# Performance work log

Hardware: AMD Instinct MI355X
Metric: run time of the kernel (lower is better)

## Reference

```python
import jax, jax.numpy as jnp
import numpy as np

THRESHOLD = 1.0
TAU_H, TAU_O = 50.0, 30.0

def setup_inputs() -> dict:
    key = jax.random.key(0)
    k1, k2, k3, k4, k5, k6 = jax.random.split(key, 6)
    B, T, S, H = 2048, 1024, 64, 256
    return {
        "sensor_history": jax.random.uniform(k1, (B, T, S), dtype=jnp.float32),
        "noise": jax.random.uniform(k2, (B, T, S), dtype=jnp.float32),
        "W_h": jax.random.normal(k3, (H, S), dtype=jnp.float32) * (1.0 / np.sqrt(S)),
        "b_h": jax.random.normal(k4, (H,), dtype=jnp.float32) * 0.01,
        "W_o": jax.random.normal(k5, (1, H), dtype=jnp.float32) * (1.0 / np.sqrt(H)),
        "b_o": jax.random.normal(k6, (1,), dtype=jnp.float32) * 0.01,
    }

def reference(sensor_history, noise, W_h, b_h, W_o, b_o):
    B, T, S = sensor_history.shape
    beta_h = jnp.exp(jnp.float32(-1.0 / TAU_H))  # membrane decay, hidden
    beta_o = jnp.exp(jnp.float32(-1.0 / TAU_O))  # membrane decay, output

    def step(carry, xs):
        v_h, v_o, acc = carry
        sensor_t, noise_t = xs  # (B, S) each
        # stochastic rate coding: spike if uniform < sensor value
        spikes_in = (noise_t < sensor_t).astype(jnp.float32)
        # hidden LIF: leaky integrate, threshold, hard reset
        v_h = beta_h * v_h + spikes_in @ W_h.T + b_h
        s_h = (v_h >= THRESHOLD).astype(jnp.float32)
        v_h = v_h * (1.0 - s_h)
        # output LIF
        v_o = beta_o * v_o + s_h @ W_o.T + b_o
        s_o = (v_o >= THRESHOLD).astype(jnp.float32)
        v_o = v_o * (1.0 - s_o)
        return (v_h, v_o, acc + s_o), None

    v_h0 = jnp.zeros((B, W_h.shape[0]), dtype=jnp.float32)
    v_o0 = jnp.zeros((B, 1), dtype=jnp.float32)
    acc0 = jnp.zeros((B, 1), dtype=jnp.float32)
    # time-major scan over the recurrence
    xs = (jnp.swapaxes(sensor_history, 0, 1), jnp.swapaxes(noise, 0, 1))
    (_, _, acc), _ = jax.lax.scan(step, (v_h0, v_o0, acc0), xs)
    return acc / jnp.float32(T)
```

## Files before the change

### kernel.cpp

```cpp
#include <hip/hip_runtime.h>

#define TT 1024
#define SS 64
#define HH 256
#define BB 4
#define TC 16
#define NC (TT / TC)

typedef _Float16 f16x8 __attribute__((ext_vector_type(8)));
typedef float    f32x4 __attribute__((ext_vector_type(4)));
typedef unsigned int u32x4 __attribute__((ext_vector_type(4)));

template <int CTRL>
__device__ __forceinline__ float dpp_add(float x) {
    int v = __float_as_int(x);
    int m = __builtin_amdgcn_update_dpp(v, v, CTRL, 0xF, 0xF, true);
    return x + __int_as_float(m);
}
__device__ __forceinline__ float wxsum_row(float x) {
    x = dpp_add<0x124>(x);
    x = dpp_add<0x128>(x);
    return x;
}

__device__ __forceinline__ float rowsum16_asm(float x) {
    float a, b, c, d;
    asm("s_nop 1\n\t"
        "v_add_f32_dpp %0, %1, %1 quad_perm:[1,0,3,2] row_mask:0xf bank_mask:0xf"
        : "=v"(a) : "v"(x));
    asm("s_nop 1\n\t"
        "v_add_f32_dpp %0, %1, %1 quad_perm:[2,3,0,1] row_mask:0xf bank_mask:0xf"
        : "=v"(b) : "v"(a));
    asm("s_nop 1\n\t"
        "v_add_f32_dpp %0, %1, %1 row_half_mirror row_mask:0xf bank_mask:0xf"
        : "=v"(c) : "v"(b));
    asm("s_nop 1\n\t"
        "v_add_f32_dpp %0, %1, %1 row_mirror row_mask:0xf bank_mask:0xf"
        : "=v"(d) : "v"(c));
    return d;
}

__launch_bounds__(512, 4)
__global__ void snn_fused(const float* __restrict__ sensor,
                          const float* __restrict__ noise,
                          const float* __restrict__ Wh,
                          const float* __restrict__ bh,
                          const float* __restrict__ Wo,
                          const float* __restrict__ bo,
                          float* __restrict__ out)
{
    __shared__ __align__(16) char  spk[2][4 * 16 * 128];
    __shared__ __align__(16) float rpart[2][BB][8][TC];

    const int tid  = threadIdx.x;
    const int lane = tid & 63;
    const int wave = tid >> 6;
    const int b0   = blockIdx.x * BB;

    f16x8 whi[2][2], wlo[2][2];
    #pragma unroll
    for (int nti = 0; nti < 2; ++nti) {
        const int h = (wave + nti * 8) * 16 + (lane & 15);
        #pragma unroll
        for (int kh = 0; kh < 2; ++kh) {
            const int k = kh * 32 + (lane >> 4) * 8;
            const float* p = Wh + (size_t)h * SS + k;
            float4 wa = *(const float4*)(p);
            float4 wb = *(const float4*)(p + 4);
            float wv[8] = {wa.x, wa.y, wa.z, wa.w, wb.x, wb.y, wb.z, wb.w};
            f16x8 fh, fl;
            #pragma unroll
            for (int j = 0; j < 8; ++j) {
                _Float16 hi = (_Float16)wv[j];
                float r1 = wv[j] - (float)hi;
                fh[j] = hi;
                fl[j] = (_Float16)(r1 * 2048.0f);
            }
            whi[nti][kh] = fh; wlo[nti][kh] = fl;
        }
    }

    const int hc = lane & 15;
    const float bh0 = bh[wave * 16 + hc], bh1 = bh[128 + wave * 16 + hc];
    const float wo0 = Wo[wave * 16 + hc], wo1 = Wo[128 + wave * 16 + hc];
    const float bov = bo[0];
    const float betah = expf(-1.0f / 50.0f);
    const float betao = expf(-1.0f / 30.0f);

    const f32x4 zero4 = {0.0f, 0.0f, 0.0f, 0.0f};

    float vh0 = 0.0f, vh1 = 0.0f;
    float vo = 0.0f, acc = 0.0f;

    const int wtw  = tid >> 7;
    const int wm   = (tid >> 3) & 15;
    const int woct = tid & 7;
    const int wrow = wtw * 16 + wm;
    const int wbyte = wrow * 128 + ((woct * 16) ^ ((wrow & 7) << 4));
    const float* sgp = sensor + ((size_t)(b0 + (wm >> 2)) * TT + wtw * 4 + (wm & 3)) * SS + woct * 8;
    const float* ngp = noise  + ((size_t)(b0 + (wm >> 2)) * TT + wtw * 4 + (wm & 3)) * SS + woct * 8;

    float4 sA, sB, nA, nB;

    auto pack_spk = [&](char* dst) {
        u32x4 sv;
        sv[0] = (nA.x < sA.x ? 0x3C00u : 0u) | (nA.y < sA.y ? 0x3C000000u : 0u);
        sv[1] = (nA.z < sA.z ? 0x3C00u : 0u) | (nA.w < sA.w ? 0x3C000000u : 0u);
        sv[2] = (nB.x < sB.x ? 0x3C00u : 0u) | (nB.y < sB.y ? 0x3C000000u : 0u);
        sv[3] = (nB.z < sB.z ? 0x3C00u : 0u) | (nB.w < sB.w ? 0x3C000000u : 0u);
        *(u32x4*)(dst + wbyte) = sv;
    };

    auto p4_step = [&](const float (*rp)[TC]) {
        const int wx  = (lane >> 2) & 7;
        const int twq = lane & 3;
        float4 q = *(const float4*)&rp[wx][twq * 4];
        q.x = wxsum_row(q.x); q.x += __shfl_xor(q.x, 16);
        q.y = wxsum_row(q.y); q.y += __shfl_xor(q.y, 16);
        q.z = wxsum_row(q.z); q.z += __shfl_xor(q.z, 16);
        q.w = wxsum_row(q.w); q.w += __shfl_xor(q.w, 16);
        #pragma unroll
        for (int ph = 0; ph < 4; ++ph) {
            if ((lane & 3) == ph) {
                float so;
                vo = (betao * vo + q.x) + bov; so = (vo >= 1.0f) ? 1.0f : 0.0f; vo = (vo >= 1.0f) ? 0.0f : vo; acc += so;
                vo = (betao * vo + q.y) + bov; so = (vo >= 1.0f) ? 1.0f : 0.0f; vo = (vo >= 1.0f) ? 0.0f : vo; acc += so;
                vo = (betao * vo + q.z) + bov; so = (vo >= 1.0f) ? 1.0f : 0.0f; vo = (vo >= 1.0f) ? 0.0f : vo; acc += so;
                vo = (betao * vo + q.w) + bov; so = (vo >= 1.0f) ? 1.0f : 0.0f; vo = (vo >= 1.0f) ? 0.0f : vo; acc += so;
            }
            vo  = __shfl(vo, ph);
            acc = __shfl(acc, ph);
        }
    };

    sA = *(const float4*)(sgp);     sB = *(const float4*)(sgp + 4);
    nA = *(const float4*)(ngp);     nB = *(const float4*)(ngp + 4);
    pack_spk(spk[0]);
    {
        const float* ps = sgp + (size_t)1 * TC * SS;
        const float* pn = ngp + (size_t)1 * TC * SS;
        sA = *(const float4*)(ps);  sB = *(const float4*)(ps + 4);
        nA = *(const float4*)(pn);  nB = *(const float4*)(pn + 4);
    }
    __syncthreads();

    const int abase = hc * 128;
    const int koff0 = (((lane >> 4)    ) * 16) ^ ((hc & 7) << 4);
    const int koff1 = (((lane >> 4) + 4) * 16) ^ ((hc & 7) << 4);

    for (int c = 0; c < NC; ++c) {
        const int cur = c & 1;

        if (c + 1 < NC) pack_spk(spk[cur ^ 1]);

        if (c + 2 < NC) {
            const float* ps = sgp + (size_t)(c + 2) * TC * SS;
            const float* pn = ngp + (size_t)(c + 2) * TC * SS;
            sA = *(const float4*)(ps);  sB = *(const float4*)(ps + 4);
            nA = *(const float4*)(pn);  nB = *(const float4*)(pn + 4);
        }

        if (c > 0 && wave < 4) p4_step(rpart[cur ^ 1][wave]);

        const char* sp = spk[cur];
        f16x8 a0 = *(const f16x8*)(sp + abase + koff0);
        f16x8 a1 = *(const f16x8*)(sp + abase + koff1);
        #pragma unroll
        for (int tw = 0; tw < 4; ++tw) {
            f16x8 n0, n1;
            if (tw < 3) {
                const char* np = sp + abase + (tw + 1) * 2048;
                n0 = *(const f16x8*)(np + koff0);
                n1 = *(const f16x8*)(np + koff1);
            } else { n0 = a0; n1 = a1; }

            f32x4 ah0 = __builtin_amdgcn_mfma_f32_16x16x32_f16(a0, whi[0][0], zero4, 0, 0, 0);
            ah0       = __builtin_amdgcn_mfma_f32_16x16x32_f16(a1, whi[0][1], ah0,   0, 0, 0);
            f32x4 al0 = __builtin_amdgcn_mfma_f32_16x16x32_f16(a0, wlo[0][0], zero4, 0, 0, 0);
            al0       = __builtin_amdgcn_mfma_f32_16x16x32_f16(a1, wlo[0][1], al0,   0, 0, 0);
            f32x4 ah1 = __builtin_amdgcn_mfma_f32_16x16x32_f16(a0, whi[1][0], zero4, 0, 0, 0);
            ah1       = __builtin_amdgcn_mfma_f32_16x16x32_f16(a1, whi[1][1], ah1,   0, 0, 0);
            f32x4 al1 = __builtin_amdgcn_mfma_f32_16x16x32_f16(a0, wlo[1][0], zero4, 0, 0, 0);
            al1       = __builtin_amdgcn_mfma_f32_16x16x32_f16(a1, wlo[1][1], al1,   0, 0, 0);

            float rcv[4];
            #pragma unroll
            for (int r = 0; r < 4; ++r) {
                const float d0 = __builtin_fmaf(al0[r], 0x1p-11f, ah0[r]);
                const float d1 = __builtin_fmaf(al1[r], 0x1p-11f, ah1[r]);
                vh0 = __builtin_fmaf(betah, vh0, d0) + bh0;
                vh1 = __builtin_fmaf(betah, vh1, d1) + bh1;
                const bool c0 = (vh0 >= 1.0f);
                const bool c1 = (vh1 >= 1.0f);
                const float rr = (c0 ? wo0 : 0.0f) + (c1 ? wo1 : 0.0f);
                vh0 = c0 ? 0.0f : vh0;
                vh1 = c1 ? 0.0f : vh1;
                rcv[r] = rowsum16_asm(rr);
            }
            if ((lane & 15) == 0) {
                float4 rq = make_float4(rcv[0], rcv[1], rcv[2], rcv[3]);
                *(float4*)&rpart[cur][lane >> 4][wave][tw * 4] = rq;
            }
            a0 = n0; a1 = n1;
        }

        __syncthreads();
    }

    if (wave < 4) {
        p4_step(rpart[(NC - 1) & 1][wave]);
        if (lane == 0) out[b0 + wave] = acc * (1.0f / (float)TT);
    }
}

extern "C" void kernel_launch(void* const* d_in, const int* in_sizes, int n_in,
                              void* d_out, int out_size, void* d_ws, size_t ws_size,
                              hipStream_t stream)
{
    const float* sensor = (const float*)d_in[0];
    const float* noise  = (const float*)d_in[1];
    const float* Wh     = (const float*)d_in[2];
    const float* bh     = (const float*)d_in[3];
    const float* Wo     = (const float*)d_in[4];
    const float* bo     = (const float*)d_in[5];
    float* out = (float*)d_out;

    const int B = in_sizes[0] / (TT * SS);
    dim3 grid(B / BB), block(512);
    hipLaunchKernelGGL(snn_fused, grid, block, 0, stream,
                       sensor, noise, Wh, bh, Wo, bo, out);
}
```

Before: 245.9 us.

## Double block to 1024 threads, one hidden tile per wave

The block grows from 8 to 16 waves. Each wave now owns a single 16-neuron hidden tile, where before it owned two, which halves the MFMA and LIF work per wave and halves the sensor/noise load per thread. The partial-sum buffer and the output-layer reduction gain an extra shuffle level to cover 16 waves. The idea is to raise parallelism and hide latency. The cost is that barriers now synchronize more waves, launch bounds allow fewer registers per thread, and the A-fragment software prefetch is removed.

After: 280.9 us. +14.2%, slower.

```diff
diff --git a/kernel.cpp b/kernel.cpp
--- a/kernel.cpp
+++ b/kernel.cpp
@@ -9,7 +9,7 @@
 
 typedef _Float16 f16x8 __attribute__((ext_vector_type(8)));
 typedef float    f32x4 __attribute__((ext_vector_type(4)));
-typedef unsigned int u32x4 __attribute__((ext_vector_type(4)));
+typedef unsigned int u32x2 __attribute__((ext_vector_type(2)));
 
 template <int CTRL>
 __device__ __forceinline__ float dpp_add(float x) {
@@ -22,7 +22,6 @@
     x = dpp_add<0x128>(x);
     return x;
 }
-
 __device__ __forceinline__ float rowsum16_asm(float x) {
     float a, b, c, d;
     asm("s_nop 1\n\t"
@@ -40,7 +39,7 @@
     return d;
 }
 
-__launch_bounds__(512, 4)
+__launch_bounds__(1024, 8)
 __global__ void snn_fused(const float* __restrict__ sensor,
                           const float* __restrict__ noise,
                           const float* __restrict__ Wh,
@@ -50,17 +49,17 @@
                           float* __restrict__ out)
 {
     __shared__ __align__(16) char  spk[2][4 * 16 * 128];
-    __shared__ __align__(16) float rpart[2][BB][8][TC];
+    __shared__ __align__(16) float rpart[2][BB][16][TC];
 
     const int tid  = threadIdx.x;
     const int lane = tid & 63;
     const int wave = tid >> 6;
     const int b0   = blockIdx.x * BB;
-
-    f16x8 whi[2][2], wlo[2][2];
-    #pragma unroll
-    for (int nti = 0; nti < 2; ++nti) {
-        const int h = (wave + nti * 8) * 16 + (lane & 15);
+    const int hc   = lane & 15;
+
+    f16x8 whi[2], wlo[2];
+    {
+        const int h = wave * 16 + hc;
         #pragma unroll
         for (int kh = 0; kh < 2; ++kh) {
             const int k = kh * 32 + (lane >> 4) * 8;
@@ -76,49 +75,45 @@
                 fh[j] = hi;
                 fl[j] = (_Float16)(r1 * 2048.0f);
             }
-            whi[nti][kh] = fh; wlo[nti][kh] = fl;
+            whi[kh] = fh; wlo[kh] = fl;
         }
     }
 
-    const int hc = lane & 15;
-    const float bh0 = bh[wave * 16 + hc], bh1 = bh[128 + wave * 16 + hc];
-    const float wo0 = Wo[wave * 16 + hc], wo1 = Wo[128 + wave * 16 + hc];
+    const float bhv = bh[wave * 16 + hc];
+    const float wov = Wo[wave * 16 + hc];
     const float bov = bo[0];
     const float betah = expf(-1.0f / 50.0f);
     const float betao = expf(-1.0f / 30.0f);
-
     const f32x4 zero4 = {0.0f, 0.0f, 0.0f, 0.0f};
 
-    float vh0 = 0.0f, vh1 = 0.0f;
+    float vh = 0.0f;
     float vo = 0.0f, acc = 0.0f;
 
-    const int wtw  = tid >> 7;
-    const int wm   = (tid >> 3) & 15;
-    const int woct = tid & 7;
-    const int wrow = wtw * 16 + wm;
-    const int wbyte = wrow * 128 + ((woct * 16) ^ ((wrow & 7) << 4));
-    const float* sgp = sensor + ((size_t)(b0 + (wm >> 2)) * TT + wtw * 4 + (wm & 3)) * SS + woct * 8;
-    const float* ngp = noise  + ((size_t)(b0 + (wm >> 2)) * TT + wtw * 4 + (wm & 3)) * SS + woct * 8;
-
-    float4 sA, sB, nA, nB;
+    const int srow = tid >> 4;
+    const int sq   = tid & 15;
+    const int stw  = srow >> 4;
+    const int sm   = srow & 15;
+    const int wbyte = srow * 128 + ((sq * 8) ^ ((srow & 7) << 4));
+    const float* sgp = sensor + ((size_t)(b0 + (sm >> 2)) * TT + stw * 4 + (sm & 3)) * SS + sq * 4;
+    const float* ngp = noise  + ((size_t)(b0 + (sm >> 2)) * TT + stw * 4 + (sm & 3)) * SS + sq * 4;
+
+    float4 sA, nA;
 
     auto pack_spk = [&](char* dst) {
-        u32x4 sv;
+        u32x2 sv;
         sv[0] = (nA.x < sA.x ? 0x3C00u : 0u) | (nA.y < sA.y ? 0x3C000000u : 0u);
         sv[1] = (nA.z < sA.z ? 0x3C00u : 0u) | (nA.w < sA.w ? 0x3C000000u : 0u);
-        sv[2] = (nB.x < sB.x ? 0x3C00u : 0u) | (nB.y < sB.y ? 0x3C000000u : 0u);
-        sv[3] = (nB.z < sB.z ? 0x3C00u : 0u) | (nB.w < sB.w ? 0x3C000000u : 0u);
-        *(u32x4*)(dst + wbyte) = sv;
+        *(u32x2*)(dst + wbyte) = sv;
     };
 
     auto p4_step = [&](const float (*rp)[TC]) {
-        const int wx  = (lane >> 2) & 7;
+        const int wx  = lane >> 2;
         const int twq = lane & 3;
         float4 q = *(const float4*)&rp[wx][twq * 4];
-        q.x = wxsum_row(q.x); q.x += __shfl_xor(q.x, 16);
-        q.y = wxsum_row(q.y); q.y += __shfl_xor(q.y, 16);
-        q.z = wxsum_row(q.z); q.z += __shfl_xor(q.z, 16);
-        q.w = wxsum_row(q.w); q.w += __shfl_xor(q.w, 16);
+        q.x = wxsum_row(q.x); q.x += __shfl_xor(q.x, 16); q.x += __shfl_xor(q.x, 32);
+        q.y = wxsum_row(q.y); q.y += __shfl_xor(q.y, 16); q.y += __shfl_xor(q.y, 32);
+        q.z = wxsum_row(q.z); q.z += __shfl_xor(q.z, 16); q.z += __shfl_xor(q.z, 32);
+        q.w = wxsum_row(q.w); q.w += __shfl_xor(q.w, 16); q.w += __shfl_xor(q.w, 32);
         #pragma unroll
         for (int ph = 0; ph < 4; ++ph) {
             if ((lane & 3) == ph) {
@@ -133,15 +128,11 @@
         }
     };
 
-    sA = *(const float4*)(sgp);     sB = *(const float4*)(sgp + 4);
-    nA = *(const float4*)(ngp);     nB = *(const float4*)(ngp + 4);
+    sA = *(const float4*)(sgp);
+    nA = *(const float4*)(ngp);
     pack_spk(spk[0]);
-    {
-        const float* ps = sgp + (size_t)1 * TC * SS;
-        const float* pn = ngp + (size_t)1 * TC * SS;
-        sA = *(const float4*)(ps);  sB = *(const float4*)(ps + 4);
-        nA = *(const float4*)(pn);  nB = *(const float4*)(pn + 4);
-    }
+    sA = *(const float4*)(sgp + (size_t)1 * TC * SS);
+    nA = *(const float4*)(ngp + (size_t)1 * TC * SS);
     __syncthreads();
 
     const int abase = hc * 128;
@@ -154,54 +145,38 @@
         if (c + 1 < NC) pack_spk(spk[cur ^ 1]);
 
         if (c + 2 < NC) {
-            const float* ps = sgp + (size_t)(c + 2) * TC * SS;
-            const float* pn = ngp + (size_t)(c + 2) * TC * SS;
-            sA = *(const float4*)(ps);  sB = *(const float4*)(ps + 4);
-            nA = *(const float4*)(pn);  nB = *(const float4*)(pn + 4);
+            sA = *(const float4*)(sgp + (size_t)(c + 2) * TC * SS);
+            nA = *(const float4*)(ngp + (size_t)(c + 2) * TC * SS);
         }
 
         if (c > 0 && wave < 4) p4_step(rpart[cur ^ 1][wave]);
 
         const char* sp = spk[cur];
-        f16x8 a0 = *(const f16x8*)(sp + abase + koff0);
-        f16x8 a1 = *(const f16x8*)(sp + abase + koff1);
         #pragma unroll
         for (int tw = 0; tw < 4; ++tw) {
-            f16x8 n0, n1;
-            if (tw < 3) {
-                const char* np = sp + abase + (tw + 1) * 2048;
-                n0 = *(const f16x8*)(np + koff0);
-                n1 = *(const f16x8*)(np + koff1);
-            } else { n0 = a0; n1 = a1; }
-
-            f32x4 ah0 = __builtin_amdgcn_mfma_f32_16x16x32_f16(a0, whi[0][0], zero4, 0, 0, 0);
-            ah0       = __builtin_amdgcn_mfma_f32_16x16x32_f16(a1, whi[0][1], ah0,   0, 0, 0);
-            f32x4 al0 = __builtin_amdgcn_mfma_f32_16x16x32_f16(a0, wlo[0][0], zero4, 0, 0, 0);
-            al0       = __builtin_amdgcn_mfma_f32_16x16x32_f16(a1, wlo[0][1], al0,   0, 0, 0);
-            f32x4 ah1 = __builtin_amdgcn_mfma_f32_16x16x32_f16(a0, whi[1][0], zero4, 0, 0, 0);
-            ah1       = __builtin_amdgcn_mfma_f32_16x16x32_f16(a1, whi[1][1], ah1,   0, 0, 0);
-            f32x4 al1 = __builtin_amdgcn_mfma_f32_16x16x32_f16(a0, wlo[1][0], zero4, 0, 0, 0);
-            al1       = __builtin_amdgcn_mfma_f32_16x16x32_f16(a1, wlo[1][1], al1,   0, 0, 0);
+            const char* np = sp + abase + tw * 2048;
+            f16x8 a0 = *(const f16x8*)(np + koff0);
+            f16x8 a1 = *(const f16x8*)(np + koff1);
+
+            f32x4 ah = __builtin_amdgcn_mfma_f32_16x16x32_f16(a0, whi[0], zero4, 0, 0, 0);
+            ah       = __builtin_amdgcn_mfma_f32_16x16x32_f16(a1, whi[1], ah,    0, 0, 0);
+            f32x4 al = __builtin_amdgcn_mfma_f32_16x16x32_f16(a0, wlo[0], zero4, 0, 0, 0);
+            al       = __builtin_amdgcn_mfma_f32_16x16x32_f16(a1, wlo[1], al,    0, 0, 0);
 
             float rcv[4];
             #pragma unroll
             for (int r = 0; r < 4; ++r) {
-                const float d0 = __builtin_fmaf(al0[r], 0x1p-11f, ah0[r]);
-                const float d1 = __builtin_fmaf(al1[r], 0x1p-11f, ah1[r]);
-                vh0 = __builtin_fmaf(betah, vh0, d0) + bh0;
-                vh1 = __builtin_fmaf(betah, vh1, d1) + bh1;
-                const bool c0 = (vh0 >= 1.0f);
-                const bool c1 = (vh1 >= 1.0f);
-                const float rr = (c0 ? wo0 : 0.0f) + (c1 ? wo1 : 0.0f);
-                vh0 = c0 ? 0.0f : vh0;
-                vh1 = c1 ? 0.0f : vh1;
+                const float d = __builtin_fmaf(al[r], 0x1p-11f, ah[r]);
+                vh = __builtin_fmaf(betah, vh, d) + bhv;
+                const bool cz = (vh >= 1.0f);
+                const float rr = cz ? wov : 0.0f;
+                vh = cz ? 0.0f : vh;
                 rcv[r] = rowsum16_asm(rr);
             }
-            if ((lane & 15) == 0) {
+            if (hc == 0) {
                 float4 rq = make_float4(rcv[0], rcv[1], rcv[2], rcv[3]);
                 *(float4*)&rpart[cur][lane >> 4][wave][tw * 4] = rq;
             }
-            a0 = n0; a1 = n1;
         }
 
         __syncthreads();
@@ -226,7 +201,7 @@
     float* out = (float*)d_out;
 
     const int B = in_sizes[0] / (TT * SS);
-    dim3 grid(B / BB), block(512);
+    dim3 grid(B / BB), block(1024);
     hipLaunchKernelGGL(snn_fused, grid, block, 0, stream,
                        sensor, noise, Wh, bh, Wo, bo, out);
 }
```
